# Performance work log

Hardware: AMD Instinct MI355X
Metric: run time of the kernel (lower is better)

## Reference

```python
import jax, jax.numpy as jnp
import numpy as np

N = 50000   # nodes
E = 800000  # edges (avg degree 16)
D = 64      # input_nf = output_nf = hidden_nf


def lrelu(x):
    # nn.LeakyReLU(0.2)
    return jnp.where(x >= 0, x, 0.2 * x)


def setup_inputs() -> dict:
    key = jax.random.key(0)
    ks = jax.random.split(key, 12)
    def lin(k, fan_in, fan_out):
        s = 1.0 / np.sqrt(fan_in)
        return jax.random.uniform(k, (fan_in, fan_out), jnp.float32, -s, s)
    inp = {
        "h": jax.random.normal(ks[0], (N, D), jnp.float32),
        "coord": jax.random.normal(ks[1], (N, 3), jnp.float32),
        "edge_index": jax.random.randint(ks[2], (2, E), 0, N, jnp.int32),
        # edge_mlp: Linear(2D+1, D) -> lrelu -> Linear(D, D) -> lrelu
        "w1e": lin(ks[3], 2 * D + 1, D), "b1e": jnp.zeros((D,), jnp.float32),
        "w2e": lin(ks[4], D, D),         "b2e": jnp.zeros((D,), jnp.float32),
        # node_mlp: Linear(2D, D) -> lrelu -> Linear(D, D)
        "w1n": lin(ks[5], 2 * D, D),     "b1n": jnp.zeros((D,), jnp.float32),
        "w2n": lin(ks[6], D, D),         "b2n": jnp.zeros((D,), jnp.float32),
    }
    return inp


def reference(h, coord, edge_index, w1e, b1e, w2e, b2e, w1n, b1n, w2n, b2n):
    row, col = edge_index[0], edge_index[1]
    # coord2radial
    coord_diff = coord[row] - coord[col]                    # [E, 3]
    radial = jnp.sum(coord_diff ** 2, axis=1, keepdims=True)  # [E, 1]
    # edge_model: concat(h[row], h[col], radial) -> MLP
    e_in = jnp.concatenate([h[row], h[col], radial], axis=1)  # [E, 2D+1]
    e = lrelu(e_in @ w1e + b1e)
    edge_feat = lrelu(e @ w2e + b2e)                        # [E, D]
    # node_model: unsorted_segment_sum over row, then MLP, residual
    agg = jax.ops.segment_sum(edge_feat, row, num_segments=N)  # [N, D]
    n_in = jnp.concatenate([h, agg], axis=1)                # [N, 2D]
    out = lrelu(n_in @ w1n + b1n) @ w2n + b2n               # [N, D]
    h_out = h + out                                         # residual=True
    # coords_weight == 0.0 -> coord passes through unchanged
    return (h_out, coord, edge_feat)
```

## Files before the change

### kernel.cpp

```cpp
#include <hip/hip_runtime.h>

#define NN 50000
#define NE 800000
#define D 64
#define SCAN_B 1024
#define NB ((NN + SCAN_B - 1) / SCAN_B)
#define TILES 5
#define EPB (64 * TILES)

typedef __attribute__((ext_vector_type(8))) short bf16x8;
typedef __attribute__((ext_vector_type(4))) float f32x4;
typedef __attribute__((ext_vector_type(4))) unsigned int u32x4;

__device__ __forceinline__ float lrelu(float x) { return x >= 0.0f ? x : 0.2f * x; }

__device__ __forceinline__ unsigned short f2bf(float f) {
    unsigned int x = __float_as_uint(f);
    unsigned int r = (x + 0x7fffu + ((x >> 16) & 1u)) >> 16;
    return (unsigned short)r;
}

__global__ __launch_bounds__(256) void prep_count(const float* __restrict__ h,
                                                  unsigned short* __restrict__ hb,
                                                  const int* __restrict__ ei,
                                                  int* __restrict__ counts,
                                                  const float* __restrict__ w1e,
                                                  const float* __restrict__ w2e,
                                                  const float* __restrict__ w1n,
                                                  const float* __restrict__ w2n,
                                                  unsigned short* __restrict__ w1t,
                                                  unsigned short* __restrict__ w2t,
                                                  unsigned short* __restrict__ w1nt,
                                                  unsigned short* __restrict__ w2nt)
{
    int i = blockIdx.x * 256 + threadIdx.x;
    float4 v = ((const float4*)h)[i];
    ushort4 o;
    o.x = f2bf(v.x); o.y = f2bf(v.y); o.z = f2bf(v.z); o.w = f2bf(v.w);
    ((ushort4*)hb)[i] = o;
    atomicAdd(&counts[ei[i]], 1);
    if (i < 8192) {
        int j = i >> 7, k = i & 127;
        w1t[i] = f2bf(w1e[k * 64 + j]);
    } else if (i < 12288) {
        int t2 = i - 8192;
        int j = t2 >> 6, k = t2 & 63;
        w2t[t2] = f2bf(w2e[k * 64 + j]);
    } else if (i < 20480) {
        int t3 = i - 12288;
        int j = t3 >> 7, k = t3 & 127;
        w1nt[t3] = f2bf(w1n[k * 64 + j]);
    } else if (i < 24576) {
        int t4 = i - 20480;
        int j = t4 >> 6, k = t4 & 63;
        w2nt[t4] = f2bf(w2n[k * 64 + j]);
    }
}

__global__ __launch_bounds__(SCAN_B) void scan_block_kernel(const int* __restrict__ counts,
                                                            int* __restrict__ offs,
                                                            int* __restrict__ bsums)
{
    int i = blockIdx.x * SCAN_B + threadIdx.x;
    int v = (i < NN) ? counts[i] : 0;
    int lane = threadIdx.x & 63;
    int wid = threadIdx.x >> 6;
    int x = v;
#pragma unroll
    for (int d = 1; d < 64; d <<= 1) {
        int y = __shfl_up(x, d);
        if (lane >= d) x += y;
    }
    __shared__ int wsum[16];
    if (lane == 63) wsum[wid] = x;
    __syncthreads();
    if (wid == 0) {
        int s = (lane < 16) ? wsum[lane] : 0;
#pragma unroll
        for (int d = 1; d < 16; d <<= 1) {
            int y = __shfl_up(s, d);
            if (lane >= d) s += y;
        }
        if (lane < 16) wsum[lane] = s;
    }
    __syncthreads();
    int woff = (wid == 0) ? 0 : wsum[wid - 1];
    int excl = woff + x - v;
    if (i < NN) offs[i] = excl;
    if (threadIdx.x == 0) bsums[blockIdx.x] = wsum[15];
}

__global__ void scan_top_kernel(int* __restrict__ bsums)
{
    if (threadIdx.x == 0 && blockIdx.x == 0) {
        int run = 0;
        for (int b = 0; b < NB; b++) { int t = bsums[b]; bsums[b] = run; run += t; }
    }
}

__global__ __launch_bounds__(SCAN_B) void add_back_kernel(int* __restrict__ offs,
                                                          const int* __restrict__ bsums,
                                                          int* __restrict__ cursor)
{
    int i = blockIdx.x * SCAN_B + threadIdx.x;
    if (i < NN) {
        int o = offs[i] + bsums[blockIdx.x];
        offs[i] = o;
        cursor[i] = o;
    }
}

__global__ __launch_bounds__(256) void scatter_kernel(const int* __restrict__ ei,
                                                      int* __restrict__ cursor,
                                                      int* __restrict__ csr,
                                                      int* __restrict__ rowpos,
                                                      int* __restrict__ colv)
{
    int e = blockIdx.x * 256 + threadIdx.x;
    if (e < NE) {
        int r = ei[e];
        int pos = atomicAdd(&cursor[r], 1);
        csr[pos] = e;
        rowpos[pos] = r;
        colv[pos] = ei[NE + e];
    }
}

__global__ __launch_bounds__(256) void egnn_edge_mfma(
    const unsigned short* __restrict__ hb, const float* __restrict__ coord,
    const int* __restrict__ csr, const int* __restrict__ rowpos,
    const int* __restrict__ colv,
    const unsigned short* __restrict__ w1t, const float* __restrict__ b1e,
    const float* __restrict__ w1e,
    const unsigned short* __restrict__ w2t, const float* __restrict__ b2e,
    float* __restrict__ edge_feat, float* __restrict__ agg)
{
    __shared__ unsigned short Alds[64 * 128];
    __shared__ unsigned short Mlds[64 * 64];
    __shared__ float rad_lds[64];
    __shared__ int rl_lds[64];
    __shared__ int el_lds[64];

    const int t = threadIdx.x;
    const int orig = blockIdx.x;
    const int xcd = orig & 7, idx8 = orig >> 3;
    const int blk = (xcd < 4 ? xcd * 313 : 4 * 313 + (xcd - 4) * 312) + idx8;

    const int lane = t & 63, wv = t >> 6;
    const int lo = lane & 15, hi = lane >> 4;

    bf16x8 b1f[4], b2f[2];
#pragma unroll
    for (int kc = 0; kc < 4; kc++)
        b1f[kc] = *(const bf16x8*)(w1t + (wv * 16 + lo) * 128 + kc * 32 + hi * 8);
#pragma unroll
    for (int kc = 0; kc < 2; kc++)
        b2f[kc] = *(const bf16x8*)(w2t + (wv * 16 + lo) * 64 + kc * 32 + hi * 8);
    const float bj1 = b1e[wv * 16 + lo];
    const float wl1 = w1e[128 * 64 + wv * 16 + lo];
    const float bj2 = b2e[wv * 16 + lo];

    const int ep = t >> 2, seg = t & 3;
    char* abase = (char*)Alds;
    char* mbase = (char*)Mlds;
    const int sw = (ep & 7) << 4;
    const int rbase = ep * 256 + seg * 64;
    const int pbase = blk * EPB;

    int e5[TILES], row5[TILES], col5[TILES];
#pragma unroll
    for (int tl = 0; tl < TILES; tl++) {
        int p = pbase + tl * 64 + ep;
        e5[tl] = csr[p];
        row5[tl] = rowpos[p];
        col5[tl] = colv[p];
    }

    float rad5[TILES];
    if (seg == 0) {
#pragma unroll
        for (int tl = 0; tl < TILES; tl++) {
            float dx = coord[row5[tl] * 3 + 0] - coord[col5[tl] * 3 + 0];
            float dy = coord[row5[tl] * 3 + 1] - coord[col5[tl] * 3 + 1];
            float dz = coord[row5[tl] * 3 + 2] - coord[col5[tl] * 3 + 2];
            rad5[tl] = dx * dx + dy * dy + dz * dz;
        }
    }

    uint4 preA[4], preB[4];
    {
        int nd0 = (seg < 2) ? row5[0] : col5[0];
        const uint4* s0 = (const uint4*)(hb + (size_t)nd0 * 64 + (seg & 1) * 32);
#pragma unroll
        for (int c = 0; c < 4; c++) preA[c] = s0[c];
        int nd1 = (seg < 2) ? row5[1] : col5[1];
        const uint4* s1 = (const uint4*)(hb + (size_t)nd1 * 64 + (seg & 1) * 32);
#pragma unroll
        for (int c = 0; c < 4; c++) preB[c] = s1[c];
    }

#pragma unroll
    for (int tl = 0; tl < TILES; tl++) {
        uint4* P = (tl & 1) ? preB : preA;
        if (tl > 0) __syncthreads();
#pragma unroll
        for (int c = 0; c < 4; c++)
            *(uint4*)(abase + ((rbase + c * 16) ^ sw)) = P[c];
        if (seg == 0) rad_lds[ep] = rad5[tl];
        if (seg == 1) rl_lds[ep] = row5[tl];
        if (seg == 2) el_lds[ep] = e5[tl];
        if (tl + 2 < TILES) {
            int nd = (seg < 2) ? row5[tl + 2] : col5[tl + 2];
            const uint4* s = (const uint4*)(hb + (size_t)nd * 64 + (seg & 1) * 32);
#pragma unroll
            for (int c = 0; c < 4; c++) P[c] = s[c];
        }
        __syncthreads();

        f32x4 acc[4];
#pragma unroll
        for (int rt = 0; rt < 4; rt++) {
#pragma unroll
            for (int r = 0; r < 4; r++)
                acc[rt][r] = fmaf(rad_lds[rt * 16 + hi * 4 + r], wl1, bj1);
        }
#pragma unroll
        for (int kc = 0; kc < 4; kc++) {
#pragma unroll
            for (int rt = 0; rt < 4; rt++) {
                int row = rt * 16 + lo;
                bf16x8 a = *(bf16x8*)(abase + ((row * 256 + kc * 64 + hi * 16) ^ ((row & 7) << 4)));
                acc[rt] = __builtin_amdgcn_mfma_f32_16x16x32_bf16(a, b1f[kc], acc[rt], 0, 0, 0);
            }
        }
#pragma unroll
        for (int rt = 0; rt < 4; rt++) {
#pragma unroll
            for (int r = 0; r < 4; r++) {
                int row = rt * 16 + hi * 4 + r;
                *(unsigned short*)(mbase + ((row * 128 + (wv * 16 + lo) * 2) ^ ((row & 7) << 4))) =
                    f2bf(lrelu(acc[rt][r]));
            }
        }
        __syncthreads();

        f32x4 acc2[4];
#pragma unroll
        for (int rt = 0; rt < 4; rt++) {
#pragma unroll
            for (int r = 0; r < 4; r++) acc2[rt][r] = bj2;
        }
#pragma unroll
        for (int kc = 0; kc < 2; kc++) {
#pragma unroll
            for (int rt = 0; rt < 4; rt++) {
                int row = rt * 16 + lo;
                bf16x8 a = *(bf16x8*)(mbase + ((row * 128 + kc * 64 + hi * 16) ^ ((row & 7) << 4)));
                acc2[rt] = __builtin_amdgcn_mfma_f32_16x16x32_bf16(a, b2f[kc], acc2[rt], 0, 0, 0);
            }
        }
#pragma unroll
        for (int rt = 0; rt < 4; rt++) {
#pragma unroll
            for (int r = 0; r < 4; r++) {
                int row = rt * 16 + hi * 4 + r;
                *(float*)(abase + ((row * 256 + (wv * 16 + lo) * 4) ^ ((row & 7) << 4))) =
                    lrelu(acc2[rt][r]);
            }
        }
        __syncthreads();

        {
            int erow4 = lane >> 4;
            int ch = lane & 15;
#pragma unroll
            for (int o = 0; o < 4; o++) {
                int ridx = wv * 16 + o * 4 + erow4;
                int ee = el_lds[ridx];
                u32x4 v = *(u32x4*)(abase + ((ridx * 256 + ch * 16) ^ ((ridx & 7) << 4)));
                __builtin_nontemporal_store(v, (u32x4*)(edge_feat + (size_t)ee * 64 + ch * 4));
            }
        }
        {
            int i0 = wv * 16;
            int cur = rl_lds[i0];
            float s = *(float*)(abase + ((i0 * 256 + lane * 4) ^ ((i0 & 7) << 4)));
#pragma unroll
            for (int ii = 1; ii < 16; ii++) {
                int idx = i0 + ii;
                int r = rl_lds[idx];
                float v = *(float*)(abase + ((idx * 256 + lane * 4) ^ ((idx & 7) << 4)));
                if (r != cur) {
                    atomicAdd(&agg[(size_t)cur * 64 + lane], s);
                    s = v; cur = r;
                } else {
                    s += v;
                }
            }
            atomicAdd(&agg[(size_t)cur * 64 + lane], s);
        }
    }
}

__global__ __launch_bounds__(256) void agg_node_mfma(
    const unsigned short* __restrict__ hb, const float* __restrict__ h,
    const float* __restrict__ coord, const float* __restrict__ agg,
    const unsigned short* __restrict__ w1nt, const float* __restrict__ b1n,
    const unsigned short* __restrict__ w2nt, const float* __restrict__ b2n,
    float* __restrict__ h_out, float* __restrict__ coord_out)
{
    __shared__ unsigned short Alds[64 * 128];
    __shared__ unsigned short Mlds[64 * 64];

    const int t = threadIdx.x, blk = blockIdx.x;
    const int lane = t & 63, wv = t >> 6;
    const int lo = lane & 15, hi = lane >> 4;
    const int nb = blk * 64;
    char* abase = (char*)Alds;
    char* mbase = (char*)Mlds;

    bf16x8 b1f[4], b2f[2];
#pragma unroll
    for (int kc = 0; kc < 4; kc++)
        b1f[kc] = *(const bf16x8*)(w1nt + (wv * 16 + lo) * 128 + kc * 32 + hi * 8);
#pragma unroll
    for (int kc = 0; kc < 2; kc++)
        b2f[kc] = *(const bf16x8*)(w2nt + (wv * 16 + lo) * 64 + kc * 32 + hi * 8);
    const float bj1 = b1n[wv * 16 + lo];
    const float bj2 = b2n[wv * 16 + lo];

    {
        int row = t >> 2, seg = t & 3;
        int n = min(nb + row, NN - 1);
        const uint4* src = (const uint4*)(hb + (size_t)n * 64 + seg * 16);
        int base = row * 256 + seg * 32;
        int swr = (row & 7) << 4;
        uint4 v0 = src[0], v1 = src[1];
        *(uint4*)(abase + (base ^ swr)) = v0;
        *(uint4*)(abase + ((base + 16) ^ swr)) = v1;
    }
    {
        int row = t >> 2, seg = t & 3;
        int n = min(nb + row, NN - 1);
        const float4* asrc = (const float4*)(agg + (size_t)n * 64 + seg * 16);
        float4 a0 = asrc[0], a1 = asrc[1], a2 = asrc[2], a3 = asrc[3];
        unsigned int u0 = f2bf(a0.x) | ((unsigned)f2bf(a0.y) << 16);
        unsigned int u1 = f2bf(a0.z) | ((unsigned)f2bf(a0.w) << 16);
        unsigned int u2 = f2bf(a1.x) | ((unsigned)f2bf(a1.y) << 16);
        unsigned int u3 = f2bf(a1.z) | ((unsigned)f2bf(a1.w) << 16);
        unsigned int u4 = f2bf(a2.x) | ((unsigned)f2bf(a2.y) << 16);
        unsigned int u5 = f2bf(a2.z) | ((unsigned)f2bf(a2.w) << 16);
        unsigned int u6 = f2bf(a3.x) | ((unsigned)f2bf(a3.y) << 16);
        unsigned int u7 = f2bf(a3.z) | ((unsigned)f2bf(a3.w) << 16);
        int base = row * 256 + 128 + seg * 32;
        int swr = (row & 7) << 4;
        *(uint4*)(abase + (base ^ swr)) = make_uint4(u0, u1, u2, u3);
        *(uint4*)(abase + ((base + 16) ^ swr)) = make_uint4(u4, u5, u6, u7);
    }
    __syncthreads();

    f32x4 acc[4];
#pragma unroll
    for (int rt = 0; rt < 4; rt++) {
#pragma unroll
        for (int r = 0; r < 4; r++) acc[rt][r] = bj1;
    }
#pragma unroll
    for (int kc = 0; kc < 4; kc++) {
#pragma unroll
        for (int rt = 0; rt < 4; rt++) {
            int row = rt * 16 + lo;
            bf16x8 a = *(bf16x8*)(abase + ((row * 256 + kc * 64 + hi * 16) ^ ((row & 7) << 4)));
            acc[rt] = __builtin_amdgcn_mfma_f32_16x16x32_bf16(a, b1f[kc], acc[rt], 0, 0, 0);
        }
    }
#pragma unroll
    for (int rt = 0; rt < 4; rt++) {
#pragma unroll
        for (int r = 0; r < 4; r++) {
            int row = rt * 16 + hi * 4 + r;
            *(unsigned short*)(mbase + ((row * 128 + (wv * 16 + lo) * 2) ^ ((row & 7) << 4))) =
                f2bf(lrelu(acc[rt][r]));
        }
    }
    __syncthreads();

    f32x4 acc2[4];
#pragma unroll
    for (int rt = 0; rt < 4; rt++) {
#pragma unroll
        for (int r = 0; r < 4; r++) acc2[rt][r] = bj2;
    }
#pragma unroll
    for (int kc = 0; kc < 2; kc++) {
#pragma unroll
        for (int rt = 0; rt < 4; rt++) {
            int row = rt * 16 + lo;
            bf16x8 a = *(bf16x8*)(mbase + ((row * 128 + kc * 64 + hi * 16) ^ ((row & 7) << 4)));
            acc2[rt] = __builtin_amdgcn_mfma_f32_16x16x32_bf16(a, b2f[kc], acc2[rt], 0, 0, 0);
        }
    }
#pragma unroll
    for (int rt = 0; rt < 4; rt++) {
#pragma unroll
        for (int r = 0; r < 4; r++) {
            int row = rt * 16 + hi * 4 + r;
            int n = nb + row;
            if (n < NN) {
                int c = wv * 16 + lo;
                float v = h[(size_t)n * 64 + c] + acc2[rt][r];
                __builtin_nontemporal_store(v, h_out + (size_t)n * 64 + c);
            }
        }
    }

    if (t < 192) {
        int idx = nb * 3 + t;
        if (idx < NN * 3) coord_out[idx] = coord[idx];
    }
}

extern "C" void kernel_launch(void* const* d_in, const int* in_sizes, int n_in,
                              void* d_out, int out_size, void* d_ws, size_t ws_size,
                              hipStream_t stream)
{
    const float* h     = (const float*)d_in[0];
    const float* coord = (const float*)d_in[1];
    const int*   ei    = (const int*)d_in[2];
    const float* w1e   = (const float*)d_in[3];
    const float* b1e   = (const float*)d_in[4];
    const float* w2e   = (const float*)d_in[5];
    const float* b2e   = (const float*)d_in[6];
    const float* w1n   = (const float*)d_in[7];
    const float* b1n   = (const float*)d_in[8];
    const float* w2n   = (const float*)d_in[9];
    const float* b2n   = (const float*)d_in[10];

    float* out       = (float*)d_out;
    float* h_out     = out;
    float* coord_out = out + (size_t)NN * D;
    float* edge_feat = coord_out + (size_t)NN * 3;

    char* ws = (char*)d_ws;
    unsigned short* hb   = (unsigned short*)ws;  ws += sizeof(unsigned short) * (size_t)NN * D;
    unsigned short* w1t  = (unsigned short*)ws;  ws += sizeof(unsigned short) * 64 * 128;
    unsigned short* w2t  = (unsigned short*)ws;  ws += sizeof(unsigned short) * 64 * 64;
    unsigned short* w1nt = (unsigned short*)ws;  ws += sizeof(unsigned short) * 64 * 128;
    unsigned short* w2nt = (unsigned short*)ws;  ws += sizeof(unsigned short) * 64 * 64;
    float* agg  = (float*)ws;                    ws += sizeof(float) * (size_t)NN * D;
    int* counts = (int*)ws;                      ws += sizeof(int) * NN;
    int* offs   = (int*)ws;                      ws += sizeof(int) * NN;
    int* cursor = (int*)ws;                      ws += sizeof(int) * NN;
    int* bsums  = (int*)ws;                      ws += sizeof(int) * 64;
    int* csr    = (int*)ws;                      ws += sizeof(int) * NE;
    int* rowpos = (int*)ws;                      ws += sizeof(int) * NE;
    int* colv   = (int*)ws;                      ws += sizeof(int) * NE;

    hipMemsetAsync(counts, 0, sizeof(int) * NN, stream);
    hipMemsetAsync(agg, 0, sizeof(float) * (size_t)NN * D, stream);

    prep_count<<<NE / 256, 256, 0, stream>>>(h, hb, ei, counts,
                                             w1e, w2e, w1n, w2n, w1t, w2t, w1nt, w2nt);

    scan_block_kernel<<<NB, SCAN_B, 0, stream>>>(counts, offs, bsums);
    scan_top_kernel<<<1, 64, 0, stream>>>(bsums);
    add_back_kernel<<<NB, SCAN_B, 0, stream>>>(offs, bsums, cursor);
    scatter_kernel<<<(NE + 255) / 256, 256, 0, stream>>>(ei, cursor, csr, rowpos, colv);

    egnn_edge_mfma<<<NE / EPB, 256, 0, stream>>>(
        hb, coord, csr, rowpos, colv, w1t, b1e, w1e, w2t, b2e, edge_feat, agg);

    agg_node_mfma<<<(NN + 63) / 64, 256, 0, stream>>>(
        hb, h, coord, agg, w1nt, b1n, w2nt, b2n, h_out, coord_out);
}
```

Baseline: 238.3 us.

## Restructure edge kernel to per-wave independent 16-edge tiles without block barriers

Each wave now processes its own 16-edge tiles. It loads gathered h rows straight into MFMA A-fragments from registers instead of staging them through shared LDS. Weights sit in LDS and are read as B-fragments, and per-wave scratch buffers use wave-local lgkmcnt fences instead of __syncthreads. Per-tile metadata (radial, row, edge id) is passed with shuffles rather than through LDS arrays. This removes block-wide barriers and the A-tile staging, at the cost of more LDS reads for weights each tile and a one-deep prefetch instead of two-deep.

```diff
diff --git a/kernel.cpp b/kernel.cpp
--- a/kernel.cpp
+++ b/kernel.cpp
@@ -18,6 +18,11 @@
     unsigned int x = __float_as_uint(f);
     unsigned int r = (x + 0x7fffu + ((x >> 16) & 1u)) >> 16;
     return (unsigned short)r;
+}
+
+__device__ __forceinline__ void wave_lds_fence() {
+    asm volatile("s_waitcnt lgkmcnt(0)" ::: "memory");
+    __builtin_amdgcn_sched_barrier(0);
 }
 
 __global__ __launch_bounds__(256) void prep_count(const float* __restrict__ h,
@@ -135,11 +140,10 @@
     const unsigned short* __restrict__ w2t, const float* __restrict__ b2e,
     float* __restrict__ edge_feat, float* __restrict__ agg)
 {
-    __shared__ unsigned short Alds[64 * 128];
-    __shared__ unsigned short Mlds[64 * 64];
-    __shared__ float rad_lds[64];
-    __shared__ int rl_lds[64];
-    __shared__ int el_lds[64];
+    __shared__ unsigned short W1[64 * 128];
+    __shared__ unsigned short W2[64 * 64];
+    __shared__ unsigned short Mb[4][16 * 64];
+    __shared__ float Ob[4][16 * 64];
 
     const int t = threadIdx.x;
     const int orig = blockIdx.x;
@@ -149,147 +153,136 @@
     const int lane = t & 63, wv = t >> 6;
     const int lo = lane & 15, hi = lane >> 4;
 
-    bf16x8 b1f[4], b2f[2];
-#pragma unroll
-    for (int kc = 0; kc < 4; kc++)
-        b1f[kc] = *(const bf16x8*)(w1t + (wv * 16 + lo) * 128 + kc * 32 + hi * 8);
-#pragma unroll
-    for (int kc = 0; kc < 2; kc++)
-        b2f[kc] = *(const bf16x8*)(w2t + (wv * 16 + lo) * 64 + kc * 32 + hi * 8);
-    const float bj1 = b1e[wv * 16 + lo];
-    const float wl1 = w1e[128 * 64 + wv * 16 + lo];
-    const float bj2 = b2e[wv * 16 + lo];
-
-    const int ep = t >> 2, seg = t & 3;
-    char* abase = (char*)Alds;
-    char* mbase = (char*)Mlds;
-    const int sw = (ep & 7) << 4;
-    const int rbase = ep * 256 + seg * 64;
-    const int pbase = blk * EPB;
+    for (int c = t; c < 1024; c += 256) {
+        int j = c >> 4, ci = c & 15;
+        uint4 v = *(const uint4*)(w1t + j * 128 + ci * 8);
+        *(uint4*)((char*)W1 + ((j * 256 + ci * 16) ^ ((j & 7) << 4))) = v;
+    }
+    for (int c = t; c < 512; c += 256) {
+        int j = c >> 3, ci = c & 7;
+        uint4 v = *(const uint4*)(w2t + j * 64 + ci * 8);
+        *(uint4*)((char*)W2 + ((j * 128 + ci * 16) ^ ((j & 7) << 4))) = v;
+    }
+    float bj1[4], wl1[4], bj2[4];
+#pragma unroll
+    for (int ct = 0; ct < 4; ct++) {
+        bj1[ct] = b1e[ct * 16 + lo];
+        wl1[ct] = w1e[128 * 64 + ct * 16 + lo];
+        bj2[ct] = b2e[ct * 16 + lo];
+    }
+    __syncthreads();
+
+    char* w1b = (char*)W1;
+    char* w2b = (char*)W2;
+    char* mb = (char*)Mb[wv];
+    char* ob = (char*)Ob[wv];
+
+    const int pbase = blk * EPB + wv * (16 * TILES);
 
     int e5[TILES], row5[TILES], col5[TILES];
+    float rad5[TILES];
 #pragma unroll
     for (int tl = 0; tl < TILES; tl++) {
-        int p = pbase + tl * 64 + ep;
+        int p = pbase + tl * 16 + lo;
         e5[tl] = csr[p];
         row5[tl] = rowpos[p];
         col5[tl] = colv[p];
     }
-
-    float rad5[TILES];
-    if (seg == 0) {
-#pragma unroll
-        for (int tl = 0; tl < TILES; tl++) {
-            float dx = coord[row5[tl] * 3 + 0] - coord[col5[tl] * 3 + 0];
-            float dy = coord[row5[tl] * 3 + 1] - coord[col5[tl] * 3 + 1];
-            float dz = coord[row5[tl] * 3 + 2] - coord[col5[tl] * 3 + 2];
-            rad5[tl] = dx * dx + dy * dy + dz * dz;
-        }
-    }
-
-    uint4 preA[4], preB[4];
-    {
-        int nd0 = (seg < 2) ? row5[0] : col5[0];
-        const uint4* s0 = (const uint4*)(hb + (size_t)nd0 * 64 + (seg & 1) * 32);
-#pragma unroll
-        for (int c = 0; c < 4; c++) preA[c] = s0[c];
-        int nd1 = (seg < 2) ? row5[1] : col5[1];
-        const uint4* s1 = (const uint4*)(hb + (size_t)nd1 * 64 + (seg & 1) * 32);
-#pragma unroll
-        for (int c = 0; c < 4; c++) preB[c] = s1[c];
-    }
-
 #pragma unroll
     for (int tl = 0; tl < TILES; tl++) {
-        uint4* P = (tl & 1) ? preB : preA;
-        if (tl > 0) __syncthreads();
-#pragma unroll
-        for (int c = 0; c < 4; c++)
-            *(uint4*)(abase + ((rbase + c * 16) ^ sw)) = P[c];
-        if (seg == 0) rad_lds[ep] = rad5[tl];
-        if (seg == 1) rl_lds[ep] = row5[tl];
-        if (seg == 2) el_lds[ep] = e5[tl];
-        if (tl + 2 < TILES) {
-            int nd = (seg < 2) ? row5[tl + 2] : col5[tl + 2];
-            const uint4* s = (const uint4*)(hb + (size_t)nd * 64 + (seg & 1) * 32);
-#pragma unroll
-            for (int c = 0; c < 4; c++) P[c] = s[c];
-        }
-        __syncthreads();
-
+        float dx = coord[row5[tl] * 3 + 0] - coord[col5[tl] * 3 + 0];
+        float dy = coord[row5[tl] * 3 + 1] - coord[col5[tl] * 3 + 1];
+        float dz = coord[row5[tl] * 3 + 2] - coord[col5[tl] * 3 + 2];
+        rad5[tl] = dx * dx + dy * dy + dz * dz;
+    }
+
+    uint4 aR0, aR1, aC0, aC1, nR0, nR1, nC0, nC1;
+    aR0 = *(const uint4*)(hb + (size_t)row5[0] * 64 + hi * 8);
+    aR1 = *(const uint4*)(hb + (size_t)row5[0] * 64 + 32 + hi * 8);
+    aC0 = *(const uint4*)(hb + (size_t)col5[0] * 64 + hi * 8);
+    aC1 = *(const uint4*)(hb + (size_t)col5[0] * 64 + 32 + hi * 8);
+
+#pragma unroll
+    for (int tl = 0; tl < TILES; tl++) {
+        if (tl + 1 < TILES) {
+            nR0 = *(const uint4*)(hb + (size_t)row5[tl + 1] * 64 + hi * 8);
+            nR1 = *(const uint4*)(hb + (size_t)row5[tl + 1] * 64 + 32 + hi * 8);
+            nC0 = *(const uint4*)(hb + (size_t)col5[tl + 1] * 64 + hi * 8);
+            nC1 = *(const uint4*)(hb + (size_t)col5[tl + 1] * 64 + 32 + hi * 8);
+        }
+
+        float radr[4];
+#pragma unroll
+        for (int r = 0; r < 4; r++) radr[r] = __shfl(rad5[tl], hi * 4 + r);
         f32x4 acc[4];
 #pragma unroll
-        for (int rt = 0; rt < 4; rt++) {
-#pragma unroll
-            for (int r = 0; r < 4; r++)
-                acc[rt][r] = fmaf(rad_lds[rt * 16 + hi * 4 + r], wl1, bj1);
-        }
+        for (int ct = 0; ct < 4; ct++)
+#pragma unroll
+            for (int r = 0; r < 4; r++) acc[ct][r] = fmaf(radr[r], wl1[ct], bj1[ct]);
+
+        bf16x8 af0 = *reinterpret_cast<bf16x8*>(&aR0);
+        bf16x8 af1 = *reinterpret_cast<bf16x8*>(&aR1);
+        bf16x8 af2 = *reinterpret_cast<bf16x8*>(&aC0);
+        bf16x8 af3 = *reinterpret_cast<bf16x8*>(&aC1);
 #pragma unroll
         for (int kc = 0; kc < 4; kc++) {
-#pragma unroll
-            for (int rt = 0; rt < 4; rt++) {
-                int row = rt * 16 + lo;
-                bf16x8 a = *(bf16x8*)(abase + ((row * 256 + kc * 64 + hi * 16) ^ ((row & 7) << 4)));
-                acc[rt] = __builtin_amdgcn_mfma_f32_16x16x32_bf16(a, b1f[kc], acc[rt], 0, 0, 0);
-            }
-        }
-#pragma unroll
-        for (int rt = 0; rt < 4; rt++) {
+            bf16x8 a = (kc == 0) ? af0 : (kc == 1) ? af1 : (kc == 2) ? af2 : af3;
+#pragma unroll
+            for (int ct = 0; ct < 4; ct++) {
+                bf16x8 b = *(bf16x8*)(w1b + (((ct * 16 + lo) * 256 + kc * 64 + hi * 16) ^ ((lo & 7) << 4)));
+                acc[ct] = __builtin_amdgcn_mfma_f32_16x16x32_bf16(a, b, acc[ct], 0, 0, 0);
+            }
+        }
+
+#pragma unroll
+        for (int ct = 0; ct < 4; ct++)
 #pragma unroll
             for (int r = 0; r < 4; r++) {
-                int row = rt * 16 + hi * 4 + r;
-                *(unsigned short*)(mbase + ((row * 128 + (wv * 16 + lo) * 2) ^ ((row & 7) << 4))) =
-                    f2bf(lrelu(acc[rt][r]));
-            }
-        }
-        __syncthreads();
+                int row = hi * 4 + r;
+                *(unsigned short*)(mb + ((row * 128 + (ct * 16 + lo) * 2) ^ ((row & 7) << 4))) =
+                    f2bf(lrelu(acc[ct][r]));
+            }
+        wave_lds_fence();
 
         f32x4 acc2[4];
 #pragma unroll
-        for (int rt = 0; rt < 4; rt++) {
-#pragma unroll
-            for (int r = 0; r < 4; r++) acc2[rt][r] = bj2;
-        }
+        for (int ct = 0; ct < 4; ct++)
+#pragma unroll
+            for (int r = 0; r < 4; r++) acc2[ct][r] = bj2[ct];
 #pragma unroll
         for (int kc = 0; kc < 2; kc++) {
-#pragma unroll
-            for (int rt = 0; rt < 4; rt++) {
-                int row = rt * 16 + lo;
-                bf16x8 a = *(bf16x8*)(mbase + ((row * 128 + kc * 64 + hi * 16) ^ ((row & 7) << 4)));
-                acc2[rt] = __builtin_amdgcn_mfma_f32_16x16x32_bf16(a, b2f[kc], acc2[rt], 0, 0, 0);
-            }
-        }
-#pragma unroll
-        for (int rt = 0; rt < 4; rt++) {
+            bf16x8 a2 = *(bf16x8*)(mb + ((lo * 128 + kc * 64 + hi * 16) ^ ((lo & 7) << 4)));
+#pragma unroll
+            for (int ct = 0; ct < 4; ct++) {
+                bf16x8 b = *(bf16x8*)(w2b + (((ct * 16 + lo) * 128 + kc * 64 + hi * 16) ^ ((lo & 7) << 4)));
+                acc2[ct] = __builtin_amdgcn_mfma_f32_16x16x32_bf16(a2, b, acc2[ct], 0, 0, 0);
+            }
+        }
+
+#pragma unroll
+        for (int ct = 0; ct < 4; ct++)
 #pragma unroll
             for (int r = 0; r < 4; r++) {
-                int row = rt * 16 + hi * 4 + r;
-                *(float*)(abase + ((row * 256 + (wv * 16 + lo) * 4) ^ ((row & 7) << 4))) =
-                    lrelu(acc2[rt][r]);
-            }
-        }
-        __syncthreads();
-
+                int row = hi * 4 + r;
+                *(float*)(ob + ((row * 256 + (ct * 16 + lo) * 4) ^ ((row & 7) << 4))) =
+                    lrelu(acc2[ct][r]);
+            }
+        wave_lds_fence();
+
+#pragma unroll
+        for (int o = 0; o < 4; o++) {
+            int ridx = o * 4 + hi;
+            int ee = __shfl(e5[tl], ridx);
+            u32x4 v = *(u32x4*)(ob + ((ridx * 256 + lo * 16) ^ ((ridx & 7) << 4)));
+            __builtin_nontemporal_store(v, (u32x4*)(edge_feat + (size_t)ee * 64 + lo * 4));
+        }
         {
-            int erow4 = lane >> 4;
-            int ch = lane & 15;
-#pragma unroll
-            for (int o = 0; o < 4; o++) {
-                int ridx = wv * 16 + o * 4 + erow4;
-                int ee = el_lds[ridx];
-                u32x4 v = *(u32x4*)(abase + ((ridx * 256 + ch * 16) ^ ((ridx & 7) << 4)));
-                __builtin_nontemporal_store(v, (u32x4*)(edge_feat + (size_t)ee * 64 + ch * 4));
-            }
-        }
-        {
-            int i0 = wv * 16;
-            int cur = rl_lds[i0];
-            float s = *(float*)(abase + ((i0 * 256 + lane * 4) ^ ((i0 & 7) << 4)));
+            int cur = __shfl(row5[tl], 0);
+            float s = *(float*)(ob + ((lane * 4) ^ 0));
 #pragma unroll
             for (int ii = 1; ii < 16; ii++) {
-                int idx = i0 + ii;
-                int r = rl_lds[idx];
-                float v = *(float*)(abase + ((idx * 256 + lane * 4) ^ ((idx & 7) << 4)));
+                int r = __shfl(row5[tl], ii);
+                float v = *(float*)(ob + ((ii * 256 + lane * 4) ^ ((ii & 7) << 4)));
                 if (r != cur) {
                     atomicAdd(&agg[(size_t)cur * 64 + lane], s);
                     s = v; cur = r;
@@ -299,6 +292,8 @@
             }
             atomicAdd(&agg[(size_t)cur * 64 + lane], s);
         }
+
+        aR0 = nR0; aR1 = nR1; aC0 = nC0; aC1 = nC1;
     }
 }
 
```

Result: faster. 202.5 us (-15.0%).
